# Optimization experiments

Measured on AMD Instinct MI355X. Metric: run time of the kernel, lower is better.

Reference implementation:

```python
import jax, jax.numpy as jnp
import numpy as np

L, B, E, H = 2048, 2, 1024, 16
HD = E // H


def setup_inputs() -> dict:
    key = jax.random.key(0)
    ks = jax.random.split(key, 5)
    s = 0.02
    return {
        "query": jax.random.normal(ks[0], (L, B, E), jnp.float32),
        "key": jax.random.normal(ks[1], (L, B, E), jnp.float32),
        "value": jax.random.normal(ks[2], (L, B, E), jnp.float32),
        "in_proj_weight": jax.random.normal(ks[3], (3 * E, E), jnp.float32) * s,
        "in_proj_bias": jnp.zeros((3 * E,), jnp.float32),
        "out_proj_weight": jax.random.normal(ks[4], (E, E), jnp.float32) * s,
        "out_proj_bias": jnp.zeros((E,), jnp.float32),
    }


def reference(query, key, value, in_proj_weight, in_proj_bias, out_proj_weight, out_proj_bias):
    # torch nn.MultiheadAttention math, seq-first [L, B, E], causal mask
    # (attend_mode='only_attend_front': positions j > i are masked).
    w_q, w_k, w_v = jnp.split(in_proj_weight, 3, axis=0)
    b_q, b_k, b_v = jnpp_split(in_proj_bias) if False else jnp.split(in_proj_bias, 3, axis=0)
    q = query @ w_q.T + b_q            # [L, B, E]
    k = key @ w_k.T + b_k
    v = value @ w_v.T + b_v

    def heads(x):  # [L, B, E] -> [B, H, L, HD]
        return x.reshape(x.shape[0], x.shape[1], H, HD).transpose(1, 2, 0, 3)

    qh, kh, vh = heads(q), heads(k), heads(v)
    scale = 1.0 / jnp.sqrt(jnp.asarray(HD, q.dtype))
    scores = jnp.einsum("bhqd,bhkd->bhqk", qh * scale, kh)  # [B, H, L, L]
    causal = jnp.triu(jnp.ones((scores.shape[-2], scores.shape[-1]), bool), k=1)
    scores = jnp.where(causal, jnp.asarray(-jnp.inf, scores.dtype), scores)
    attn = jax.nn.softmax(scores, axis=-1)
    out = jnp.einsum("bhqk,bhkd->bhqd", attn, vh)           # [B, H, L, HD]
    out = out.transpose(2, 0, 1, 3).reshape(query.shape[0], query.shape[1], E)  # [L, B, E]
    out = out @ out_proj_weight.T + out_proj_bias
    # torch also returns head-averaged attn weights [B, L, L]
    attn_avg = attn.mean(axis=1)
    return out, attn_avg
```

## Files before the change

### kernel.cpp

```cpp
#include <hip/hip_runtime.h>

#define L_ 2048
#define B_ 2
#define E_ 1024
#define H_ 16
#define HD_ 64
#define M_ 4096
#define K_ 1024

typedef unsigned short u16;
typedef unsigned int u32;
using short8  = __attribute__((ext_vector_type(8))) short;
using short4v = __attribute__((ext_vector_type(4))) short;
using floatx4 = __attribute__((ext_vector_type(4))) float;

__device__ inline u16 f2b(float f) {
  unsigned u = __float_as_uint(f);
  u += 0x7FFF + ((u >> 16) & 1);
  return (u16)(u >> 16);
}

__device__ inline u32 pack2(float a, float b) {
  u32 ua = __float_as_uint(a) + 0x8000u;
  u32 ub = __float_as_uint(b) + 0x8000u;
  return (ua >> 16) | (ub & 0xFFFF0000u);
}

__device__ inline floatx4 mfma16(short8 a, short8 b, floatx4 c) {
  return __builtin_amdgcn_mfma_f32_16x16x32_bf16(a, b, c, 0, 0, 0);
}

__device__ inline void gload16(const void* g, void* l) {
  __builtin_amdgcn_global_load_lds(
      (const __attribute__((address_space(1))) u32*)g,
      (__attribute__((address_space(3))) u32*)l, 16, 0, 0);
}

__global__ void convall(const float* __restrict__ q, const float* __restrict__ k,
                        const float* __restrict__ v, const float* __restrict__ wi,
                        const float* __restrict__ wo,
                        u16* __restrict__ xb, u16* __restrict__ wib,
                        u16* __restrict__ wob) {
  const int z = blockIdx.z;
  const float* src;
  u16* dst;
  int n4;
  if (z < 3)      { src = (z == 0 ? q : (z == 1 ? k : v));
                    dst = xb + (size_t)z * M_ * K_; n4 = M_ * K_ / 4; }
  else if (z == 3){ src = wi; dst = wib; n4 = 3 * E_ * K_ / 4; }
  else            { src = wo; dst = wob; n4 = E_ * K_ / 4; }
  int i = blockIdx.x * blockDim.x + threadIdx.x;
  if (i < n4) {
    float4 val = ((const float4*)src)[i];
    ushort4 o;
    o.x = f2b(val.x); o.y = f2b(val.y); o.z = f2b(val.z); o.w = f2b(val.w);
    ((ushort4*)dst)[i] = o;
  }
}

template <int MODE>
__global__ __launch_bounds__(256) void gemm128(
    const u16* __restrict__ A, const u16* __restrict__ W, const float* __restrict__ bias,
    u16* __restrict__ qh, u16* __restrict__ kh, u16* __restrict__ vhT,
    float* __restrict__ outp)
{
  __shared__ __align__(16) u16 As[2][128 * 32];
  __shared__ __align__(16) u16 Bs[2][128 * 32];
  const int p = (MODE == 0) ? blockIdx.z : 0;
  const u16* Ap = A + (size_t)p * M_ * K_;
  const u16* Wp = W + (size_t)p * E_ * K_;
  const float* bp = bias + p * E_;
  const int row0 = blockIdx.y * 128, col0 = blockIdx.x * 128;
  const int t = threadIdx.x, lane = t & 63, wv = t >> 6;
  const int lanem = lane & 15, quad = lane >> 4;
  const int wm = wv >> 1, wn = wv & 1;

  int f0 = t, f1 = 256 + t;
  int r0s = f0 >> 2, q0s = (f0 & 3) ^ ((r0s >> 1) & 3);
  int r1s = f1 >> 2, q1s = (f1 & 3) ^ ((r1s >> 1) & 3);

  floatx4 acc[4][4];
#pragma unroll
  for (int mi = 0; mi < 4; ++mi)
#pragma unroll
    for (int ni = 0; ni < 4; ++ni) acc[mi][ni] = (floatx4){0.f, 0.f, 0.f, 0.f};

  const int swz = (lanem >> 1) & 3;

  auto STAGE = [&](int buf, int k0) {
    gload16(Ap + (size_t)(row0 + r0s) * K_ + k0 + q0s * 8, (char*)As[buf] + wv * 1024);
    gload16(Wp + (size_t)(col0 + r0s) * K_ + k0 + q0s * 8, (char*)Bs[buf] + wv * 1024);
    gload16(Ap + (size_t)(row0 + r1s) * K_ + k0 + q1s * 8, (char*)As[buf] + 4096 + wv * 1024);
    gload16(Wp + (size_t)(col0 + r1s) * K_ + k0 + q1s * 8, (char*)Bs[buf] + 4096 + wv * 1024);
  };

  STAGE(0, 0);
  for (int k0 = 0; k0 < K_; k0 += 32) {
    const int buf = (k0 >> 5) & 1;
    __syncthreads();
    if (k0 + 32 < K_) STAGE(buf ^ 1, k0 + 32);
    short8 af[4], bfg[4];
#pragma unroll
    for (int mi = 0; mi < 4; ++mi) {
      int r = wm * 64 + mi * 16 + lanem;
      af[mi] = *(const short8*)((const char*)As[buf] + r * 64 + (quad ^ swz) * 16);
    }
#pragma unroll
    for (int ni = 0; ni < 4; ++ni) {
      int r = wn * 64 + ni * 16 + lanem;
      bfg[ni] = *(const short8*)((const char*)Bs[buf] + r * 64 + (quad ^ swz) * 16);
    }
#pragma unroll
    for (int mi = 0; mi < 4; ++mi)
#pragma unroll
      for (int ni = 0; ni < 4; ++ni)
        acc[mi][ni] = mfma16(af[mi], bfg[ni], acc[mi][ni]);
  }

#pragma unroll
  for (int ni = 0; ni < 4; ++ni) {
    int gc = col0 + wn * 64 + ni * 16 + lanem;
    float bv = bp[gc];
#pragma unroll
    for (int mi = 0; mi < 4; ++mi) {
      int gr0 = row0 + wm * 64 + mi * 16 + quad * 4;
#pragma unroll
      for (int v = 0; v < 4; ++v) {
        float val = acc[mi][ni][v] + bv;
        int r = gr0 + v;
        if (MODE == 1) {
          outp[(size_t)r * E_ + gc] = val;
        } else {
          int l = r >> 1, bb = r & 1, hh = gc >> 6, d = gc & 63;
          u16 x = f2b(val);
          if (p == 0)      qh[(((size_t)bb * H_ + hh) * L_ + l) * HD_ + d] = x;
          else if (p == 1) kh[(((size_t)bb * H_ + hh) * L_ + l) * HD_ + d] = x;
          else {
            int lp = (l & ~31) | (((l >> 2) & 3) * 8 + ((l >> 4) & 1) * 4 + (l & 3));
            vhT[(((size_t)bb * H_ + hh) * HD_ + d) * L_ + lp] = x;
          }
        }
      }
    }
  }
}

__global__ __launch_bounds__(256, 2) void attn1(
    const u16* __restrict__ qh, const u16* __restrict__ kh, const u16* __restrict__ vhT,
    u16* __restrict__ ctx, float* __restrict__ li_ws)
{
  __shared__ __align__(16) u16 Ks[2][64 * 64];
  __shared__ __align__(16) u16 Vs[2][64 * 64];
  const int g = blockIdx.x;
  const int h = blockIdx.y, b = blockIdx.z;
  const int t = threadIdx.x, lane = t & 63, wv = t >> 6;
  const int lanem = lane & 15, quad = lane >> 4;
  const int bh = b * H_ + h;
  const int gB = (L_ / 64 - 1) - g;
  const int rowA = g * 64 + wv * 16 + lanem;
  const int rowB = gB * 64 + wv * 16 + lanem;

  const u16* qpA = qh + ((size_t)bh * L_ + rowA) * HD_;
  const u16* qpB = qh + ((size_t)bh * L_ + rowB) * HD_;
  short8 qA0 = *(const short8*)(qpA + quad * 8);
  short8 qA1 = *(const short8*)(qpA + 32 + quad * 8);
  short8 qB0 = *(const short8*)(qpB + quad * 8);
  short8 qB1 = *(const short8*)(qpB + 32 + quad * 8);

  const int srow = lane >> 3;
  const int spiece = (lane & 7) ^ srow;
  const u16* ksrc = kh + ((size_t)bh * L_ + wv * 16 + srow) * HD_ + spiece * 8;
  const u16* vsrc = vhT + ((size_t)bh * HD_ + wv * 16 + srow) * L_ + spiece * 8;

  const int ntiles = 32 - g;
  auto stage = [&](int buf) {
    gload16(ksrc, (char*)Ks[buf] + wv * 2048);
    gload16(ksrc + 8 * HD_, (char*)Ks[buf] + wv * 2048 + 1024);
    gload16(vsrc, (char*)Vs[buf] + wv * 2048);
    gload16(vsrc + (size_t)8 * L_, (char*)Vs[buf] + wv * 2048 + 1024);
    ksrc += 64 * HD_;
    vsrc += 64;
  };

  const int swz = lanem & 7;
  const int cb0 = lanem * 128 + ((quad ^ swz)) * 16;
  const int cb1 = lanem * 128 + ((quad ^ swz) ^ 4) * 16;

  float liA = 0.f, liB = 0.f;
  floatx4 oA[4], oB[4];
#pragma unroll
  for (int d = 0; d < 4; ++d) { oA[d] = (floatx4){0.f,0.f,0.f,0.f}; oB[d] = oA[d]; }

  int j0 = 0, tcur = 0;

  auto do_tile = [&](int modeA, int modeB) {
    __syncthreads();
    if (tcur + 1 < ntiles) stage((tcur + 1) & 1);
    const char* kbuf = (const char*)Ks[tcur & 1];
    const char* vbuf = (const char*)Vs[tcur & 1];

    floatx4 sA[4], sB[4];
#pragma unroll
    for (int jf = 0; jf < 4; ++jf) {
      short8 a0 = *(const short8*)(kbuf + cb0 + jf * 2048);
      short8 a1 = *(const short8*)(kbuf + cb1 + jf * 2048);
      floatx4 z = (floatx4){0.f,0.f,0.f,0.f};
      if (modeA != 2) sA[jf] = mfma16(a1, qA1, mfma16(a0, qA0, z));
      sB[jf] = mfma16(a1, qB1, mfma16(a0, qB0, z));
    }

    short8 pbA[2], pbB[2];
    auto soft = [&](floatx4* st, int row, float& li, short8* pb, int masked) {
#pragma unroll
      for (int jc = 0; jc < 2; ++jc) {
        float p[8];
#pragma unroll
        for (int r = 0; r < 4; ++r) {
          int ja = j0 + jc * 32 + quad * 4 + r;
          float e0 = __expf(st[jc * 2][r] * 0.125f);
          float e1 = __expf(st[jc * 2 + 1][r] * 0.125f);
          if (masked) {
            e0 = (ja <= row) ? e0 : 0.f;
            e1 = (ja + 16 <= row) ? e1 : 0.f;
          }
          li += e0 + e1;
          p[r] = e0; p[4 + r] = e1;
        }
        union { u32 w[4]; short8 s; } u;
        u.w[0] = pack2(p[0], p[1]); u.w[1] = pack2(p[2], p[3]);
        u.w[2] = pack2(p[4], p[5]); u.w[3] = pack2(p[6], p[7]);
        pb[jc] = u.s;
      }
    };
    if (modeA == 0) soft(sA, rowA, liA, pbA, 0);
    else if (modeA == 1) soft(sA, rowA, liA, pbA, 1);
    if (modeB == 0) soft(sB, rowB, liB, pbB, 0);
    else soft(sB, rowB, liB, pbB, 1);

#pragma unroll
    for (int jc = 0; jc < 2; ++jc) {
      const int base = (jc == 0) ? cb0 : cb1;
#pragma unroll
      for (int dbl = 0; dbl < 4; ++dbl) {
        short8 vf = *(const short8*)(vbuf + base + dbl * 2048);
        if (modeA != 2) oA[dbl] = mfma16(vf, pbA[jc], oA[dbl]);
        oB[dbl] = mfma16(vf, pbB[jc], oB[dbl]);
      }
    }
    j0 += 64;
    ++tcur;
  };

  stage(0);
  for (int jt = 0; jt < g; ++jt) do_tile(0, 0);
  do_tile(1, 0);
  for (int jt = g + 1; jt <= 30 - g; ++jt) do_tile(2, 0);
  do_tile(2, 1);

  liA += __shfl_xor(liA, 16); liA += __shfl_xor(liA, 32);
  liB += __shfl_xor(liB, 16); liB += __shfl_xor(liB, 32);
  float invA = 1.0f / liA, invB = 1.0f / liB;

  u16* cA = ctx + ((size_t)rowA * B_ + b) * E_ + h * HD_ + quad * 4;
  u16* cB = ctx + ((size_t)rowB * B_ + b) * E_ + h * HD_ + quad * 4;
#pragma unroll
  for (int dbl = 0; dbl < 4; ++dbl) {
    ushort4 pkA, pkB;
    pkA.x = f2b(oA[dbl][0] * invA); pkA.y = f2b(oA[dbl][1] * invA);
    pkA.z = f2b(oA[dbl][2] * invA); pkA.w = f2b(oA[dbl][3] * invA);
    pkB.x = f2b(oB[dbl][0] * invB); pkB.y = f2b(oB[dbl][1] * invB);
    pkB.z = f2b(oB[dbl][2] * invB); pkB.w = f2b(oB[dbl][3] * invB);
    *(ushort4*)(cA + dbl * 16) = pkA;
    *(ushort4*)(cB + dbl * 16) = pkB;
  }
  if (quad == 0) {
    li_ws[(size_t)bh * L_ + rowA] = invA;
    li_ws[(size_t)bh * L_ + rowB] = invB;
  }
}

__global__ __launch_bounds__(256) void attn2(
    const u16* __restrict__ qh, const u16* __restrict__ kh,
    const float* __restrict__ li_ws, float* __restrict__ out2)
{
  __shared__ __align__(16) u16 Ks[2][2][64 * 64];
  const int jt = blockIdx.x, it = blockIdx.y, b = blockIdx.z;
  const int t = threadIdx.x, lane = t & 63, wv = t >> 6;
  const int lanem = lane & 15, quad = lane >> 4;
  const int i0 = it * 64 + wv * 16;
  const int j0 = jt * 64;
  float* ob = out2 + (size_t)b * L_ * L_;

  if (jt > it) {
    float4 z = {0.f, 0.f, 0.f, 0.f};
    float* rp = ob + (size_t)(i0 + lanem) * L_ + j0 + quad * 16;
    ((float4*)rp)[0] = z; ((float4*)rp)[1] = z;
    ((float4*)rp)[2] = z; ((float4*)rp)[3] = z;
    return;
  }

  const int srow = lane >> 3;
  const int spiece = (lane & 7) ^ srow;
  const int swz = lanem & 7;

  auto stage = [&](int p, int buf) {
#pragma unroll
    for (int hh = 0; hh < 2; ++hh) {
      const u16* kg = kh + ((size_t)(b * H_ + 2 * p + hh) * L_ + j0) * HD_;
#pragma unroll
      for (int k = wv * 2; k < wv * 2 + 2; ++k)
        gload16(kg + (size_t)(k * 8 + srow) * HD_ + spiece * 8,
                (char*)Ks[buf][hh] + k * 1024);
    }
  };
  auto loadQ = [&](int p, short8 q[2][2], floatx4 lf[2]) {
#pragma unroll
    for (int hh = 0; hh < 2; ++hh) {
      int bh = b * H_ + 2 * p + hh;
      const u16* qb = qh + ((size_t)bh * L_ + i0 + lanem) * HD_;
      q[hh][0] = *(const short8*)(qb + quad * 8);
      q[hh][1] = *(const short8*)(qb + 32 + quad * 8);
      lf[hh] = *(const floatx4*)(li_ws + (size_t)bh * L_ + i0 + quad * 4);
    }
  };

  float acc[4][4] = {};
  short8 qc[2][2]; floatx4 lc[2];
  stage(0, 0);
  loadQ(0, qc, lc);

#pragma unroll
  for (int p = 0; p < 8; ++p) {
    const int buf = p & 1;
    __syncthreads();
    if (p < 7) stage(p + 1, 1 - buf);
    short8 qn[2][2]; floatx4 ln[2];
    loadQ(p < 7 ? p + 1 : 7, qn, ln);
#pragma unroll
    for (int hh = 0; hh < 2; ++hh) {
      const char* tb = (const char*)Ks[buf][hh];
#pragma unroll
      for (int s = 0; s < 4; ++s) {
        if (j0 + s * 16 > i0 + 15) continue;
        const char* kr = tb + (s * 16 + lanem) * 128;
        short8 b0 = *(const short8*)(kr + (quad ^ swz) * 16);
        short8 b1 = *(const short8*)(kr + ((4 + quad) ^ swz) * 16);
        floatx4 sv = (floatx4){0.f, 0.f, 0.f, 0.f};
        sv = mfma16(qc[hh][0], b0, sv);
        sv = mfma16(qc[hh][1], b1, sv);
        if (j0 + s * 16 + 15 <= i0) {
#pragma unroll
          for (int r = 0; r < 4; ++r)
            acc[s][r] += __expf(sv[r] * 0.125f) * lc[hh][r];
        } else {
#pragma unroll
          for (int r = 0; r < 4; ++r) {
            int irow = i0 + quad * 4 + r;
            int jc = j0 + s * 16 + lanem;
            if (jc <= irow) acc[s][r] += __expf(sv[r] * 0.125f) * lc[hh][r];
          }
        }
      }
    }
#pragma unroll
    for (int hh = 0; hh < 2; ++hh) {
      qc[hh][0] = qn[hh][0]; qc[hh][1] = qn[hh][1]; lc[hh] = ln[hh];
    }
  }

#pragma unroll
  for (int s = 0; s < 4; ++s)
#pragma unroll
    for (int r = 0; r < 4; ++r) {
      int irow = i0 + quad * 4 + r;
      int jc = j0 + s * 16 + lanem;
      ob[(size_t)irow * L_ + jc] = acc[s][r] * (1.0f / H_);
    }
}

extern "C" void kernel_launch(void* const* d_in, const int* in_sizes, int n_in,
                              void* d_out, int out_size, void* d_ws, size_t ws_size,
                              hipStream_t stream) {
  const float* query = (const float*)d_in[0];
  const float* key   = (const float*)d_in[1];
  const float* value = (const float*)d_in[2];
  const float* w_in  = (const float*)d_in[3];
  const float* b_in  = (const float*)d_in[4];
  const float* w_out = (const float*)d_in[5];
  const float* b_out = (const float*)d_in[6];

  char* ws = (char*)d_ws;
  size_t off = 0;
  auto alloc = [&](size_t bytes) -> void* {
    void* p = ws + off;
    off += (bytes + 255) & ~(size_t)255;
    return p;
  };
  u16* w_in_b  = (u16*)alloc((size_t)3 * E_ * K_ * 2);
  u16* w_out_b = (u16*)alloc((size_t)E_ * K_ * 2);
  u16* x_b     = (u16*)alloc((size_t)3 * M_ * K_ * 2);
  u16* qh      = (u16*)alloc((size_t)B_ * H_ * L_ * HD_ * 2);
  u16* kh      = (u16*)alloc((size_t)B_ * H_ * L_ * HD_ * 2);
  u16* vhT     = (u16*)alloc((size_t)B_ * H_ * L_ * HD_ * 2);
  u16* ctx     = (u16*)alloc((size_t)M_ * E_ * 2);
  float* li_ws = (float*)alloc((size_t)B_ * H_ * L_ * 4);

  convall<<<dim3(4096, 1, 5), 256, 0, stream>>>(
      query, key, value, w_in, w_out, x_b, w_in_b, w_out_b);

  gemm128<0><<<dim3(E_ / 128, M_ / 128, 3), 256, 0, stream>>>(
      x_b, w_in_b, b_in, qh, kh, vhT, nullptr);

  attn1<<<dim3(L_ / 128, H_, B_), 256, 0, stream>>>(qh, kh, vhT, ctx, li_ws);

  attn2<<<dim3(L_ / 64, L_ / 64, B_), 256, 0, stream>>>(
      qh, kh, li_ws, (float*)d_out + (size_t)M_ * E_);

  gemm128<1><<<dim3(E_ / 128, M_ / 128, 1), 256, 0, stream>>>(
      ctx, w_out_b, b_out, nullptr, nullptr, nullptr, (float*)d_out);
}
```

Before: 265.3 us.

## Merge attention-weight kernel and output projection GEMM into one launch

Combines the head-averaged attention-weights kernel and the output-projection GEMM into a single launch, using a third grid z-slice whose first 8x32 blocks run the GEMM while the other blocks exit immediately. The two independent workloads can then overlap on the GPU and one launch plus its tail gap is removed. The cost is a larger grid with many immediately-returning blocks and a shared-memory layout sized to whichever path needs more, which could limit occupancy.

```diff
diff --git a/kernel.cpp b/kernel.cpp
--- a/kernel.cpp
+++ b/kernel.cpp
@@ -58,15 +58,13 @@
   }
 }
 
-template <int MODE>
-__global__ __launch_bounds__(256) void gemm128(
+__global__ __launch_bounds__(256) void gemm_qkv(
     const u16* __restrict__ A, const u16* __restrict__ W, const float* __restrict__ bias,
-    u16* __restrict__ qh, u16* __restrict__ kh, u16* __restrict__ vhT,
-    float* __restrict__ outp)
+    u16* __restrict__ qh, u16* __restrict__ kh, u16* __restrict__ vhT)
 {
   __shared__ __align__(16) u16 As[2][128 * 32];
   __shared__ __align__(16) u16 Bs[2][128 * 32];
-  const int p = (MODE == 0) ? blockIdx.z : 0;
+  const int p = blockIdx.z;
   const u16* Ap = A + (size_t)p * M_ * K_;
   const u16* Wp = W + (size_t)p * E_ * K_;
   const float* bp = bias + p * E_;
@@ -128,17 +126,13 @@
       for (int v = 0; v < 4; ++v) {
         float val = acc[mi][ni][v] + bv;
         int r = gr0 + v;
-        if (MODE == 1) {
-          outp[(size_t)r * E_ + gc] = val;
-        } else {
-          int l = r >> 1, bb = r & 1, hh = gc >> 6, d = gc & 63;
-          u16 x = f2b(val);
-          if (p == 0)      qh[(((size_t)bb * H_ + hh) * L_ + l) * HD_ + d] = x;
-          else if (p == 1) kh[(((size_t)bb * H_ + hh) * L_ + l) * HD_ + d] = x;
-          else {
-            int lp = (l & ~31) | (((l >> 2) & 3) * 8 + ((l >> 4) & 1) * 4 + (l & 3));
-            vhT[(((size_t)bb * H_ + hh) * HD_ + d) * L_ + lp] = x;
-          }
+        int l = r >> 1, bb = r & 1, hh = gc >> 6, d = gc & 63;
+        u16 x = f2b(val);
+        if (p == 0)      qh[(((size_t)bb * H_ + hh) * L_ + l) * HD_ + d] = x;
+        else if (p == 1) kh[(((size_t)bb * H_ + hh) * L_ + l) * HD_ + d] = x;
+        else {
+          int lp = (l & ~31) | (((l >> 2) & 3) * 8 + ((l >> 4) & 1) * 4 + (l & 3));
+          vhT[(((size_t)bb * H_ + hh) * HD_ + d) * L_ + lp] = x;
         }
       }
     }
@@ -279,14 +273,84 @@
   }
 }
 
-__global__ __launch_bounds__(256) void attn2(
+__global__ __launch_bounds__(256) void fused_tail(
     const u16* __restrict__ qh, const u16* __restrict__ kh,
-    const float* __restrict__ li_ws, float* __restrict__ out2)
+    const float* __restrict__ li_ws, float* __restrict__ out2,
+    const u16* __restrict__ ctx, const u16* __restrict__ wo,
+    const float* __restrict__ bo, float* __restrict__ outp)
 {
-  __shared__ __align__(16) u16 Ks[2][2][64 * 64];
-  const int jt = blockIdx.x, it = blockIdx.y, b = blockIdx.z;
+  __shared__ __align__(16) u16 smem[4][64 * 64];
   const int t = threadIdx.x, lane = t & 63, wv = t >> 6;
   const int lanem = lane & 15, quad = lane >> 4;
+
+  if (blockIdx.z == 2) {
+    if (blockIdx.x >= 8) return;
+    u16* base = &smem[0][0];
+    const int row0 = blockIdx.y * 128, col0 = blockIdx.x * 128;
+    const int wm = wv >> 1, wn = wv & 1;
+
+    int f0 = t, f1 = 256 + t;
+    int r0s = f0 >> 2, q0s = (f0 & 3) ^ ((r0s >> 1) & 3);
+    int r1s = f1 >> 2, q1s = (f1 & 3) ^ ((r1s >> 1) & 3);
+
+    floatx4 acc[4][4];
+#pragma unroll
+    for (int mi = 0; mi < 4; ++mi)
+#pragma unroll
+      for (int ni = 0; ni < 4; ++ni) acc[mi][ni] = (floatx4){0.f, 0.f, 0.f, 0.f};
+
+    const int swz = (lanem >> 1) & 3;
+
+    auto STAGE = [&](int buf, int k0) {
+      u16* As = base + buf * 4096;
+      u16* Bs = base + 8192 + buf * 4096;
+      gload16(ctx + (size_t)(row0 + r0s) * K_ + k0 + q0s * 8, (char*)As + wv * 1024);
+      gload16(wo  + (size_t)(col0 + r0s) * K_ + k0 + q0s * 8, (char*)Bs + wv * 1024);
+      gload16(ctx + (size_t)(row0 + r1s) * K_ + k0 + q1s * 8, (char*)As + 4096 + wv * 1024);
+      gload16(wo  + (size_t)(col0 + r1s) * K_ + k0 + q1s * 8, (char*)Bs + 4096 + wv * 1024);
+    };
+
+    STAGE(0, 0);
+    for (int k0 = 0; k0 < K_; k0 += 32) {
+      const int buf = (k0 >> 5) & 1;
+      __syncthreads();
+      if (k0 + 32 < K_) STAGE(buf ^ 1, k0 + 32);
+      const u16* As = base + buf * 4096;
+      const u16* Bs = base + 8192 + buf * 4096;
+      short8 af[4], bfg[4];
+#pragma unroll
+      for (int mi = 0; mi < 4; ++mi) {
+        int r = wm * 64 + mi * 16 + lanem;
+        af[mi] = *(const short8*)((const char*)As + r * 64 + (quad ^ swz) * 16);
+      }
+#pragma unroll
+      for (int ni = 0; ni < 4; ++ni) {
+        int r = wn * 64 + ni * 16 + lanem;
+        bfg[ni] = *(const short8*)((const char*)Bs + r * 64 + (quad ^ swz) * 16);
+      }
+#pragma unroll
+      for (int mi = 0; mi < 4; ++mi)
+#pragma unroll
+        for (int ni = 0; ni < 4; ++ni)
+          acc[mi][ni] = mfma16(af[mi], bfg[ni], acc[mi][ni]);
+    }
+
+#pragma unroll
+    for (int ni = 0; ni < 4; ++ni) {
+      int gc = col0 + wn * 64 + ni * 16 + lanem;
+      float bv = bo[gc];
+#pragma unroll
+      for (int mi = 0; mi < 4; ++mi) {
+        int gr0 = row0 + wm * 64 + mi * 16 + quad * 4;
+#pragma unroll
+        for (int v = 0; v < 4; ++v)
+          outp[(size_t)(gr0 + v) * E_ + gc] = acc[mi][ni][v] + bv;
+      }
+    }
+    return;
+  }
+
+  const int jt = blockIdx.x, it = blockIdx.y, b = blockIdx.z;
   const int i0 = it * 64 + wv * 16;
   const int j0 = jt * 64;
   float* ob = out2 + (size_t)b * L_ * L_;
@@ -310,7 +374,7 @@
 #pragma unroll
       for (int k = wv * 2; k < wv * 2 + 2; ++k)
         gload16(kg + (size_t)(k * 8 + srow) * HD_ + spiece * 8,
-                (char*)Ks[buf][hh] + k * 1024);
+                (char*)smem[buf * 2 + hh] + k * 1024);
     }
   };
   auto loadQ = [&](int p, short8 q[2][2], floatx4 lf[2]) {
@@ -338,7 +402,7 @@
     loadQ(p < 7 ? p + 1 : 7, qn, ln);
 #pragma unroll
     for (int hh = 0; hh < 2; ++hh) {
-      const char* tb = (const char*)Ks[buf][hh];
+      const char* tb = (const char*)smem[buf * 2 + hh];
 #pragma unroll
       for (int s = 0; s < 4; ++s) {
         if (j0 + s * 16 > i0 + 15) continue;
@@ -408,14 +472,12 @@
   convall<<<dim3(4096, 1, 5), 256, 0, stream>>>(
       query, key, value, w_in, w_out, x_b, w_in_b, w_out_b);
 
-  gemm128<0><<<dim3(E_ / 128, M_ / 128, 3), 256, 0, stream>>>(
-      x_b, w_in_b, b_in, qh, kh, vhT, nullptr);
+  gemm_qkv<<<dim3(E_ / 128, M_ / 128, 3), 256, 0, stream>>>(
+      x_b, w_in_b, b_in, qh, kh, vhT);
 
   attn1<<<dim3(L_ / 128, H_, B_), 256, 0, stream>>>(qh, kh, vhT, ctx, li_ws);
 
-  attn2<<<dim3(L_ / 64, L_ / 64, B_), 256, 0, stream>>>(
-      qh, kh, li_ws, (float*)d_out + (size_t)M_ * E_);
-
-  gemm128<1><<<dim3(E_ / 128, M_ / 128, 1), 256, 0, stream>>>(
-      ctx, w_out_b, b_out, nullptr, nullptr, nullptr, (float*)d_out);
-}
+  fused_tail<<<dim3(L_ / 64, L_ / 64, 3), 256, 0, stream>>>(
+      qh, kh, li_ws, (float*)d_out + (size_t)M_ * E_,
+      ctx, w_out_b, b_out, (float*)d_out);
+}
```

Measured after the change: 330.7 us. +24.6%, slower.

## Fold softmax scale and log2e into Q projection, use exp2, single-head K staging

Applied to the files above, without the earlier changes.

Multiplies Q by scale*log2(e) in the projection epilogue, so both attention kernels can use the hardware exp2 directly without a per-element multiply. The attn2 kernel also changes from staging two heads' K tiles per iteration (8 iterations) to one head per iteration (16 iterations), which halves shared memory and the registers held for Q. The trade-off is twice as many barriers and pipeline steps in attn2, for a possible gain in occupancy. Folding the scale into bf16 Q slightly changes rounding.

```diff
diff --git a/kernel.cpp b/kernel.cpp
--- a/kernel.cpp
+++ b/kernel.cpp
@@ -29,6 +29,9 @@
 __device__ inline floatx4 mfma16(short8 a, short8 b, floatx4 c) {
   return __builtin_amdgcn_mfma_f32_16x16x32_bf16(a, b, c, 0, 0, 0);
 }
+
+__device__ inline float fexp2(float x) { return __builtin_amdgcn_exp2f(x); }
+#define QSCALE 0.1803368801111244f
 
 __device__ inline void gload16(const void* g, void* l) {
   __builtin_amdgcn_global_load_lds(
@@ -127,6 +130,7 @@
 #pragma unroll
       for (int v = 0; v < 4; ++v) {
         float val = acc[mi][ni][v] + bv;
+        if (MODE == 0 && p == 0) val *= QSCALE;
         int r = gr0 + v;
         if (MODE == 1) {
           outp[(size_t)r * E_ + gc] = val;
@@ -217,8 +221,8 @@
 #pragma unroll
         for (int r = 0; r < 4; ++r) {
           int ja = j0 + jc * 32 + quad * 4 + r;
-          float e0 = __expf(st[jc * 2][r] * 0.125f);
-          float e1 = __expf(st[jc * 2 + 1][r] * 0.125f);
+          float e0 = fexp2(st[jc * 2][r]);
+          float e1 = fexp2(st[jc * 2 + 1][r]);
           if (masked) {
             e0 = (ja <= row) ? e0 : 0.f;
             e1 = (ja + 16 <= row) ? e1 : 0.f;
@@ -283,7 +287,7 @@
     const u16* __restrict__ qh, const u16* __restrict__ kh,
     const float* __restrict__ li_ws, float* __restrict__ out2)
 {
-  __shared__ __align__(16) u16 Ks[2][2][64 * 64];
+  __shared__ __align__(16) u16 Ks[2][64 * 64];
   const int jt = blockIdx.x, it = blockIdx.y, b = blockIdx.z;
   const int t = threadIdx.x, lane = t & 63, wv = t >> 6;
   const int lanem = lane & 15, quad = lane >> 4;
@@ -303,69 +307,57 @@
   const int spiece = (lane & 7) ^ srow;
   const int swz = lanem & 7;
 
-  auto stage = [&](int p, int buf) {
-#pragma unroll
-    for (int hh = 0; hh < 2; ++hh) {
-      const u16* kg = kh + ((size_t)(b * H_ + 2 * p + hh) * L_ + j0) * HD_;
-#pragma unroll
-      for (int k = wv * 2; k < wv * 2 + 2; ++k)
-        gload16(kg + (size_t)(k * 8 + srow) * HD_ + spiece * 8,
-                (char*)Ks[buf][hh] + k * 1024);
-    }
-  };
-  auto loadQ = [&](int p, short8 q[2][2], floatx4 lf[2]) {
-#pragma unroll
-    for (int hh = 0; hh < 2; ++hh) {
-      int bh = b * H_ + 2 * p + hh;
-      const u16* qb = qh + ((size_t)bh * L_ + i0 + lanem) * HD_;
-      q[hh][0] = *(const short8*)(qb + quad * 8);
-      q[hh][1] = *(const short8*)(qb + 32 + quad * 8);
-      lf[hh] = *(const floatx4*)(li_ws + (size_t)bh * L_ + i0 + quad * 4);
-    }
+  auto stage = [&](int h, int buf) {
+    const u16* kg = kh + ((size_t)(b * H_ + h) * L_ + j0) * HD_;
+#pragma unroll
+    for (int k = wv * 2; k < wv * 2 + 2; ++k)
+      gload16(kg + (size_t)(k * 8 + srow) * HD_ + spiece * 8,
+              (char*)Ks[buf] + k * 1024);
+  };
+  auto loadQ = [&](int h, short8 q[2], floatx4& lf) {
+    int bh = b * H_ + h;
+    const u16* qb = qh + ((size_t)bh * L_ + i0 + lanem) * HD_;
+    q[0] = *(const short8*)(qb + quad * 8);
+    q[1] = *(const short8*)(qb + 32 + quad * 8);
+    lf = *(const floatx4*)(li_ws + (size_t)bh * L_ + i0 + quad * 4);
   };
 
   float acc[4][4] = {};
-  short8 qc[2][2]; floatx4 lc[2];
+  short8 qc[2]; floatx4 lc;
   stage(0, 0);
   loadQ(0, qc, lc);
 
 #pragma unroll
-  for (int p = 0; p < 8; ++p) {
+  for (int p = 0; p < 16; ++p) {
     const int buf = p & 1;
     __syncthreads();
-    if (p < 7) stage(p + 1, 1 - buf);
-    short8 qn[2][2]; floatx4 ln[2];
-    loadQ(p < 7 ? p + 1 : 7, qn, ln);
-#pragma unroll
-    for (int hh = 0; hh < 2; ++hh) {
-      const char* tb = (const char*)Ks[buf][hh];
-#pragma unroll
-      for (int s = 0; s < 4; ++s) {
-        if (j0 + s * 16 > i0 + 15) continue;
-        const char* kr = tb + (s * 16 + lanem) * 128;
-        short8 b0 = *(const short8*)(kr + (quad ^ swz) * 16);
-        short8 b1 = *(const short8*)(kr + ((4 + quad) ^ swz) * 16);
-        floatx4 sv = (floatx4){0.f, 0.f, 0.f, 0.f};
-        sv = mfma16(qc[hh][0], b0, sv);
-        sv = mfma16(qc[hh][1], b1, sv);
-        if (j0 + s * 16 + 15 <= i0) {
-#pragma unroll
-          for (int r = 0; r < 4; ++r)
-            acc[s][r] += __expf(sv[r] * 0.125f) * lc[hh][r];
-        } else {
-#pragma unroll
-          for (int r = 0; r < 4; ++r) {
-            int irow = i0 + quad * 4 + r;
-            int jc = j0 + s * 16 + lanem;
-            if (jc <= irow) acc[s][r] += __expf(sv[r] * 0.125f) * lc[hh][r];
-          }
+    if (p < 15) stage(p + 1, buf ^ 1);
+    short8 qn[2]; floatx4 ln;
+    loadQ(p < 15 ? p + 1 : 15, qn, ln);
+    const char* tb = (const char*)Ks[buf];
+#pragma unroll
+    for (int s = 0; s < 4; ++s) {
+      if (j0 + s * 16 > i0 + 15) continue;
+      const char* kr = tb + (s * 16 + lanem) * 128;
+      short8 b0 = *(const short8*)(kr + (quad ^ swz) * 16);
+      short8 b1 = *(const short8*)(kr + ((4 + quad) ^ swz) * 16);
+      floatx4 sv = (floatx4){0.f, 0.f, 0.f, 0.f};
+      sv = mfma16(qc[0], b0, sv);
+      sv = mfma16(qc[1], b1, sv);
+      if (j0 + s * 16 + 15 <= i0) {
+#pragma unroll
+        for (int r = 0; r < 4; ++r)
+          acc[s][r] += fexp2(sv[r]) * lc[r];
+      } else {
+#pragma unroll
+        for (int r = 0; r < 4; ++r) {
+          int irow = i0 + quad * 4 + r;
+          int jc = j0 + s * 16 + lanem;
+          if (jc <= irow) acc[s][r] += fexp2(sv[r]) * lc[r];
         }
       }
     }
-#pragma unroll
-    for (int hh = 0; hh < 2; ++hh) {
-      qc[hh][0] = qn[hh][0]; qc[hh][1] = qn[hh][1]; lc[hh] = ln[hh];
-    }
+    qc[0] = qn[0]; qc[1] = qn[1]; lc = ln;
   }
 
 #pragma unroll
```

Result: no change. 265.0 us (-0.1%).
